# Kernel tuning notes

Measured on AMD Instinct MI355X. Metric: run time of the kernel, lower is better.

## Reference

```python
import jax, jax.numpy as jnp
import numpy as np

NP, NA, H, K, TAU = 4096, 2048, 128, 5, 1.0
NODE_N = {'paper': NP, 'author': NA}
RELS = [('pp', 'paper', 'paper'), ('aa', 'author', 'author'),
        ('pa', 'paper', 'author'), ('ap', 'author', 'paper')]


def setup_inputs():
    key = jax.random.key(0)
    ks = jax.random.split(key, 32)
    f32 = jnp.float32
    def nrm(k, shape, scale=1.0):
        return jax.random.normal(k, shape, f32) * scale
    Epp, Eaa, Epa, Eap = 131072, 65536, 131072, 131072
    inp = {
        'x_paper': nrm(ks[0], (NP, H)),
        'x_author': nrm(ks[1], (NA, H)),
        'ei_pp': jax.random.randint(ks[2], (2, Epp), 0, NP, dtype=jnp.int32),
        'ei_aa': jax.random.randint(ks[3], (2, Eaa), 0, NA, dtype=jnp.int32),
        'ei_pa': jnp.stack([jax.random.randint(ks[4], (Epa,), 0, NP, dtype=jnp.int32),
                            jax.random.randint(ks[5], (Epa,), 0, NA, dtype=jnp.int32)]),
        'ei_ap': jnp.stack([jax.random.randint(ks[6], (Eap,), 0, NA, dtype=jnp.int32),
                            jax.random.randint(ks[7], (Eap,), 0, NP, dtype=jnp.int32)]),
        'batch_paper': jnp.zeros((NP,), jnp.int32),
        'batch_author': jnp.zeros((NA,), jnp.int32),
        'index': 7,
    }
    s = H ** -0.5
    i = 8
    for t in ('paper', 'author'):
        for l in (0, 1):
            inp['Wself_%s%d' % (t, l)] = nrm(ks[i], (H, H), s); i += 1
    for r, _, _ in RELS:
        for l in (0, 1):
            inp['W%s%d' % (r, l)] = nrm(ks[i], (H, H), s); i += 1
    for r in ('pp', 'aa'):
        inp['Wep1_%s' % r] = nrm(ks[i], (2 * H, 256), (2 * H) ** -0.5); i += 1
        inp['bep1_%s' % r] = jnp.zeros((256,), f32)
        inp['Wep2_%s' % r] = nrm(ks[i], (256, 2), 256 ** -0.5); i += 1
        inp['bep2_%s' % r] = jnp.zeros((2,), f32)
    inp['Wc'] = nrm(ks[i], (H, 5), s)
    inp['bc'] = jnp.zeros((5,), f32)
    return inp


def _mean_agg(msg, dst, n):
    s = jax.ops.segment_sum(msg, dst, num_segments=n)
    c = jax.ops.segment_sum(jnp.ones((msg.shape[0], 1), msg.dtype), dst, num_segments=n)
    return s / jnp.maximum(c, 1.0)


def _gnn(x, ei, p, single, edge_attn=None):
    # 2-layer relation-typed mean-aggregation hetero GNN.
    h = dict(x)
    for l in (0, 1):
        nh = {}
        for t in ('paper', 'author'):
            agg = h[t] @ p['Wself_%s%d' % (t, l)]
            for r, s_t, d_t in RELS:
                if d_t != t or (single and s_t != d_t):
                    continue
                src, dst = ei[r][0], ei[r][1]
                msg = h[s_t][src] @ p['W%s%d' % (r, l)]  # [E, H]
                if edge_attn is not None and r in edge_attn:
                    msg = msg * edge_attn[r][:, None]
                agg = agg + _mean_agg(msg, dst, NODE_N[t])
            nh[t] = jax.nn.relu(agg)
        h = nh
    return h


def _edge_pred(h, ei, p, r, t):
    src, dst = ei[r][0], ei[r][1]
    e = jnp.concatenate([h[t][src], h[t][dst]], axis=-1)  # [E, 2H]
    e = jax.nn.relu(e @ p['Wep1_%s' % r] + p['bep1_%s' % r])
    return e @ p['Wep2_%s' % r] + p['bep2_%s' % r]  # [E, 2]


def _gumbel_topk(logits, mask, k, tau, key):
    # Masked straight-through top-k gumbel-softmax (row-wise, hard=True).
    u = jax.random.uniform(key, logits.shape, logits.dtype, 1e-10, 1.0)
    g = -jnp.log(-jnp.log(u))
    y = jnp.where(mask, (logits + g) / tau, -1e9)
    soft = jax.nn.softmax(y, axis=-1)
    _, idx = jax.lax.top_k(soft, k)  # [N, k]
    rows = jnp.arange(logits.shape[0])[:, None]
    hard = jnp.zeros_like(soft).at[rows, idx].set(1.0)
    return hard - jax.lax.stop_gradient(soft) + soft


def _prune(h, ei, p, r, t, n, key):
    pred = _edge_pred(h, ei, p, r, t)[:, 0]
    src, dst = ei[r][0], ei[r][1]
    # sparse_coo_tensor(...).to_dense(): duplicates coalesce by sum
    A = jnp.zeros((n, n), pred.dtype).at[src, dst].add(pred)
    S = _gumbel_topk(A, A > 0, K, TAU, key)
    return S[src, dst]


def _forward(p, ints):
    x = {'paper': p['x_paper'], 'author': p['x_author']}
    ei = {'pp': ints['ei_pp'], 'aa': ints['ei_aa'], 'pa': ints['ei_pa'], 'ap': ints['ei_ap']}
    h1 = _gnn(x, ei, p, single=True)
    kpp, kaa = jax.random.split(jax.random.key(42))
    w_pp = _prune(h1, ei, p, 'pp', 'paper', NP, kpp)
    w_aa = _prune(h1, ei, p, 'aa', 'author', NA, kaa)
    h2 = _gnn(x, ei, p, single=False, edge_attn={'pp': w_pp, 'aa': w_aa})
    pool = h2['paper'][ints['index']].reshape(1, -1)
    y_hat = pool @ p['Wc'] + p['bc']
    return y_hat, w_pp, w_aa


def reference(x_paper, x_author, ei_pp, ei_aa, ei_pa, ei_ap, batch_paper, batch_author, index,
              Wself_paper0, Wself_paper1, Wself_author0, Wself_author1,
              Wpp0, Wpp1, Waa0, Waa1, Wpa0, Wpa1, Wap0, Wap1,
              Wep1_pp, bep1_pp, Wep2_pp, bep2_pp, Wep1_aa, bep1_aa, Wep2_aa, bep2_aa,
              Wc, bc):
    p = dict(x_paper=x_paper, x_author=x_author,
             Wself_paper0=Wself_paper0, Wself_paper1=Wself_paper1,
             Wself_author0=Wself_author0, Wself_author1=Wself_author1,
             Wpp0=Wpp0, Wpp1=Wpp1, Waa0=Waa0, Waa1=Waa1,
             Wpa0=Wpa0, Wpa1=Wpa1, Wap0=Wap0, Wap1=Wap1,
             Wep1_pp=Wep1_pp, bep1_pp=bep1_pp, Wep2_pp=Wep2_pp, bep2_pp=bep2_pp,
             Wep1_aa=Wep1_aa, bep1_aa=bep1_aa, Wep2_aa=Wep2_aa, bep2_aa=bep2_aa,
             Wc=Wc, bc=bc)
    ints = dict(ei_pp=ei_pp, ei_aa=ei_aa, ei_pa=ei_pa, ei_ap=ei_ap, index=index)
    return _forward(p, ints)
```

## Files before the change

kernel.cpp:

```cpp
#include <hip/hip_runtime.h>
#include <stdint.h>


namespace {

constexpr int NPn = 4096;
constexpr int NAn = 2048;
constexpr int Hh  = 128;
constexpr int EPPc = 131072;
constexpr int EAAc = 65536;
constexpr int KSEL = 5;
constexpr int BSLOT = 128;


__host__ __device__ static inline void tf2x32(uint32_t k0, uint32_t k1,
                                              uint32_t& x0, uint32_t& x1) {
  uint32_t ks2 = k0 ^ k1 ^ 0x1BD11BDAu;
  x0 += k0; x1 += k1;
#define TF_R(r) { x0 += x1; x1 = (x1 << (r)) | (x1 >> (32 - (r))); x1 ^= x0; }
  TF_R(13) TF_R(15) TF_R(26) TF_R(6)
  x0 += k1;  x1 += ks2 + 1u;
  TF_R(17) TF_R(29) TF_R(16) TF_R(24)
  x0 += ks2; x1 += k0 + 2u;
  TF_R(13) TF_R(15) TF_R(26) TF_R(6)
  x0 += k0;  x1 += k1 + 3u;
  TF_R(17) TF_R(29) TF_R(16) TF_R(24)
  x0 += k1;  x1 += ks2 + 4u;
  TF_R(13) TF_R(15) TF_R(26) TF_R(6)
  x0 += ks2; x1 += k0 + 5u;
#undef TF_R
}

__global__ __launch_bounds__(256) void scatter_kernel(
    const int* src_pp, const int* dst_pp, const int* src_aa, const int* dst_aa,
    const int* src_pa, const int* dst_pa, const int* src_ap, const int* dst_ap,
    int* cnt, int* entries)
{
  int i = blockIdx.x * 256 + threadIdx.x;
  int key, pl;
  if (i < 131072) {
    int e = i;
    key = 0 + dst_pp[e]; pl = (src_pp[e] << 18) | e;
  } else if (i < 196608) {
    int e = i - 131072;
    key = 4096 + dst_aa[e]; pl = (src_aa[e] << 16) | e;
  } else if (i < 327680) {
    int e = i - 196608;
    key = 6144 + dst_pa[e]; pl = src_pa[e];
  } else if (i < 458752) {
    int e = i - 327680;
    key = 8192 + dst_ap[e]; pl = src_ap[e];
  } else if (i < 589824) {
    int e = i - 458752;
    key = 12288 + src_pp[e]; pl = (dst_pp[e] << 18) | e;
  } else if (i < 655360) {
    int e = i - 589824;
    key = 16384 + src_aa[e]; pl = (dst_aa[e] << 16) | e;
  } else return;
  int pos = atomicAdd(&cnt[key], 1);
  if (pos < BSLOT) entries[key * BSLOT + pos] = pl;
}

struct FDesc {
  const float* gsrc; const float* wArr; int cntOff; int shift;
  float* Mout;
  const float* Aself; const float* W0; const float* W1;
  const float* A2;  const float* W2;
  float* C; int relu;
  const float* WP; float* P1; float* P2;
};
struct FArgs { FDesc d[4]; int bstart[5]; int nd; };

__global__ __launch_bounds__(256) void fused_layer(FArgs fa, const int* __restrict__ cnt,
                                                   const int* __restrict__ entries)
{
  __shared__ __align__(16) float Ms[8][128];
  __shared__ __align__(16) float Xs[8][128];
  __shared__ __align__(16) float Zs[8][128];
  __shared__ __align__(16) float Ws[32][128];
  int blk = blockIdx.x, tid = threadIdx.x;
  int di = 0;
  while (di < fa.nd - 1 && blk >= fa.bstart[di + 1]) ++di;
  FDesc D = fa.d[di];
  int node0 = (blk - fa.bstart[di]) * 8;
  {
    int hw = tid >> 5;
    int node = node0 + hw;
    int fl = (tid & 31) << 2;
    int deg = cnt[D.cntOff + node];
    const int* ent = entries + (size_t)(D.cntOff + node) * BSLOT;
    const float* h = D.gsrc;
    int sh = D.shift;
    float ax = 0.f, ay = 0.f, az = 0.f, aw = 0.f;
    if (D.wArr) {
      unsigned mask = (1u << sh) - 1u;
      int k = 0;
      for (; k + 3 < deg; k += 4) {
        unsigned p0 = (unsigned)ent[k], p1 = (unsigned)ent[k + 1];
        unsigned p2 = (unsigned)ent[k + 2], p3 = (unsigned)ent[k + 3];
        float w0 = D.wArr[p0 & mask], w1 = D.wArr[p1 & mask];
        float w2v = D.wArr[p2 & mask], w3 = D.wArr[p3 & mask];
        float4 v0, v1, v2, v3;
        if (w0 != 0.f) v0 = *(const float4*)&h[(size_t)(p0 >> sh) * Hh + fl];
        if (w1 != 0.f) v1 = *(const float4*)&h[(size_t)(p1 >> sh) * Hh + fl];
        if (w2v != 0.f) v2 = *(const float4*)&h[(size_t)(p2 >> sh) * Hh + fl];
        if (w3 != 0.f) v3 = *(const float4*)&h[(size_t)(p3 >> sh) * Hh + fl];
        if (w0 != 0.f) { ax += v0.x; ay += v0.y; az += v0.z; aw += v0.w; }
        if (w1 != 0.f) { ax += v1.x; ay += v1.y; az += v1.z; aw += v1.w; }
        if (w2v != 0.f) { ax += v2.x; ay += v2.y; az += v2.z; aw += v2.w; }
        if (w3 != 0.f) { ax += v3.x; ay += v3.y; az += v3.z; aw += v3.w; }
      }
      for (; k < deg; ++k) {
        unsigned pl = (unsigned)ent[k];
        float wt = D.wArr[pl & mask];
        if (wt != 0.f) {
          float4 v = *(const float4*)&h[(size_t)(pl >> sh) * Hh + fl];
          ax += v.x; ay += v.y; az += v.z; aw += v.w;
        }
      }
    } else {
      int k = 0;
      for (; k + 7 < deg; k += 8) {
        unsigned p0 = (unsigned)ent[k],     p1 = (unsigned)ent[k + 1];
        unsigned p2 = (unsigned)ent[k + 2], p3 = (unsigned)ent[k + 3];
        unsigned p4 = (unsigned)ent[k + 4], p5 = (unsigned)ent[k + 5];
        unsigned p6 = (unsigned)ent[k + 6], p7 = (unsigned)ent[k + 7];
        float4 v0 = *(const float4*)&h[(size_t)(p0 >> sh) * Hh + fl];
        float4 v1 = *(const float4*)&h[(size_t)(p1 >> sh) * Hh + fl];
        float4 v2 = *(const float4*)&h[(size_t)(p2 >> sh) * Hh + fl];
        float4 v3 = *(const float4*)&h[(size_t)(p3 >> sh) * Hh + fl];
        float4 v4 = *(const float4*)&h[(size_t)(p4 >> sh) * Hh + fl];
        float4 v5 = *(const float4*)&h[(size_t)(p5 >> sh) * Hh + fl];
        float4 v6 = *(const float4*)&h[(size_t)(p6 >> sh) * Hh + fl];
        float4 v7 = *(const float4*)&h[(size_t)(p7 >> sh) * Hh + fl];
        ax += v0.x; ay += v0.y; az += v0.z; aw += v0.w;
        ax += v1.x; ay += v1.y; az += v1.z; aw += v1.w;
        ax += v2.x; ay += v2.y; az += v2.z; aw += v2.w;
        ax += v3.x; ay += v3.y; az += v3.z; aw += v3.w;
        ax += v4.x; ay += v4.y; az += v4.z; aw += v4.w;
        ax += v5.x; ay += v5.y; az += v5.z; aw += v5.w;
        ax += v6.x; ay += v6.y; az += v6.z; aw += v6.w;
        ax += v7.x; ay += v7.y; az += v7.z; aw += v7.w;
      }
      for (; k < deg; ++k) {
        unsigned pl = (unsigned)ent[k];
        float4 v = *(const float4*)&h[(size_t)(pl >> sh) * Hh + fl];
        ax += v.x; ay += v.y; az += v.z; aw += v.w;
      }
    }
    float cd = fmaxf((float)deg, 1.0f);
    float4 o; o.x = ax / cd; o.y = ay / cd; o.z = az / cd; o.w = aw / cd;
    if (D.W0 == nullptr) {
      *(float4*)&D.Mout[(size_t)node * Hh + fl] = o;
    } else {
      *(float4*)&Ms[hw][fl] = o;
    }
  }
  if (D.W0 == nullptr) return;
  {
    int rm = tid >> 5, cq = (tid & 31) << 2;
    *(float4*)&Xs[rm][cq] = *(const float4*)&D.Aself[(size_t)(node0 + rm) * 128 + cq];
    if (D.A2)
      *(float4*)&Zs[rm][cq] = *(const float4*)&D.A2[(size_t)(node0 + rm) * 128 + cq];
  }
  int m = tid >> 5, nq = tid & 31;
  float4 accv = {0.f, 0.f, 0.f, 0.f};
  int parts = D.A2 ? 3 : 2;
  for (int p = 0; p < parts; ++p) {
    const float* W = (p == 0) ? D.W0 : (p == 1) ? D.W1 : D.W2;
    for (int c = 0; c < 4; ++c) {
      __syncthreads();
      {
        int r = tid >> 3, f = (tid & 7) << 4;
        const float* srcp = &W[(size_t)(c * 32 + r) * 128 + f];
        *(float4*)&Ws[r][f]      = *(const float4*)&srcp[0];
        *(float4*)&Ws[r][f + 4]  = *(const float4*)&srcp[4];
        *(float4*)&Ws[r][f + 8]  = *(const float4*)&srcp[8];
        *(float4*)&Ws[r][f + 12] = *(const float4*)&srcp[12];
      }
      __syncthreads();
#define KCHUNK(AR)                                              \
      _Pragma("unroll")                                         \
      for (int k = 0; k < 32; ++k) {                            \
        float a = AR[m][c * 32 + k];                            \
        float4 wv = *(const float4*)&Ws[k][nq << 2];            \
        accv.x += a * wv.x; accv.y += a * wv.y;                 \
        accv.z += a * wv.z; accv.w += a * wv.w;                 \
      }
      if (p == 0) { KCHUNK(Xs) } else if (p == 1) { KCHUNK(Ms) } else { KCHUNK(Zs) }
#undef KCHUNK
    }
  }
  if (D.relu) {
    accv.x = fmaxf(accv.x, 0.f); accv.y = fmaxf(accv.y, 0.f);
    accv.z = fmaxf(accv.z, 0.f); accv.w = fmaxf(accv.w, 0.f);
  }
  if (D.C)
    *(float4*)&D.C[(size_t)(node0 + m) * 128 + (nq << 2)] = accv;
  if (D.WP == nullptr) return;
  __syncthreads();
  *(float4*)&Xs[m][nq << 2] = accv;
  __syncthreads();
  {
    int half = tid >> 7;
    int rg = (tid >> 6) & 1;
    int c0 = (tid & 63) << 2;
    const float* Wb = D.WP + ((size_t)(half ? 128 : 0)) * 256 + c0;
    float4 acc0 = {0,0,0,0}, acc1 = {0,0,0,0}, acc2 = {0,0,0,0}, acc3 = {0,0,0,0};
    for (int k = 0; k < 128; k += 2) {
      float4 w0 = *(const float4*)&Wb[(size_t)k * 256];
      float4 w1 = *(const float4*)&Wb[(size_t)(k + 1) * 256];
      float2 a0 = *(const float2*)&Xs[rg * 4 + 0][k];
      float2 a1 = *(const float2*)&Xs[rg * 4 + 1][k];
      float2 a2 = *(const float2*)&Xs[rg * 4 + 2][k];
      float2 a3 = *(const float2*)&Xs[rg * 4 + 3][k];
      acc0.x += a0.x * w0.x; acc0.y += a0.x * w0.y; acc0.z += a0.x * w0.z; acc0.w += a0.x * w0.w;
      acc0.x += a0.y * w1.x; acc0.y += a0.y * w1.y; acc0.z += a0.y * w1.z; acc0.w += a0.y * w1.w;
      acc1.x += a1.x * w0.x; acc1.y += a1.x * w0.y; acc1.z += a1.x * w0.z; acc1.w += a1.x * w0.w;
      acc1.x += a1.y * w1.x; acc1.y += a1.y * w1.y; acc1.z += a1.y * w1.z; acc1.w += a1.y * w1.w;
      acc2.x += a2.x * w0.x; acc2.y += a2.x * w0.y; acc2.z += a2.x * w0.z; acc2.w += a2.x * w0.w;
      acc2.x += a2.y * w1.x; acc2.y += a2.y * w1.y; acc2.z += a2.y * w1.z; acc2.w += a2.y * w1.w;
      acc3.x += a3.x * w0.x; acc3.y += a3.x * w0.y; acc3.z += a3.x * w0.z; acc3.w += a3.x * w0.w;
      acc3.x += a3.y * w1.x; acc3.y += a3.y * w1.y; acc3.z += a3.y * w1.z; acc3.w += a3.y * w1.w;
    }
    float* Pout = half ? D.P2 : D.P1;
    *(float4*)&Pout[(size_t)(node0 + rg * 4 + 0) * 256 + c0] = acc0;
    *(float4*)&Pout[(size_t)(node0 + rg * 4 + 1) * 256 + c0] = acc1;
    *(float4*)&Pout[(size_t)(node0 + rg * 4 + 2) * 256 + c0] = acc2;
    *(float4*)&Pout[(size_t)(node0 + rg * 4 + 3) * 256 + c0] = acc3;
  }
}

__global__ __launch_bounds__(256) void row_topk(
    const float* __restrict__ P1pp, const float* __restrict__ P2pp,
    const float* __restrict__ b1pp, const float* __restrict__ W2pp,
    const float* __restrict__ b2pp,
    const float* __restrict__ P1aa, const float* __restrict__ P2aa,
    const float* __restrict__ b1aa, const float* __restrict__ W2aa,
    const float* __restrict__ b2aa,
    const int* __restrict__ cnt, const int* __restrict__ entries,
    float* __restrict__ w_pp, float* __restrict__ w_aa,
    uint32_t kpp0, uint32_t kpp1, uint32_t kaa0, uint32_t kaa1)
{
  __shared__ int   dS[4][128];
  __shared__ float pS[4][128];
  __shared__ int   sel5[4][KSEL];
  int blk = blockIdx.x, tid = threadIdx.x;
  int lane = tid & 63, wv = tid >> 6;
  int row, Ncols, shift;
  int co; unsigned mask;
  const float* P1; const float* P2; const float* b1; const float* W2; const float* b2;
  float* wout; uint32_t k0, k1;
  if (blk < NPn / 4) {
    row = blk * 4 + wv; Ncols = NPn; shift = 18; mask = 0x3FFFFu; co = 12288;
    P1 = P1pp; P2 = P2pp; b1 = b1pp; W2 = W2pp; b2 = b2pp;
    wout = w_pp; k0 = kpp0; k1 = kpp1;
  } else {
    row = (blk - NPn / 4) * 4 + wv; Ncols = NAn; shift = 16; mask = 0xFFFFu; co = 16384;
    P1 = P1aa; P2 = P2aa; b1 = b1aa; W2 = W2aa; b2 = b2aa;
    wout = w_aa; k0 = kaa0; k1 = kaa1;
  }
  const int* ent = entries + (size_t)(co + row) * BSLOT;
  int deg = cnt[co + row];
  int j = lane << 2;
  float4 p1v = *(const float4*)&P1[(size_t)row * 256 + j];
  float4 b1v = *(const float4*)&b1[j];
  float wa = W2[(j + 0) * 2], wb = W2[(j + 1) * 2];
  float wc = W2[(j + 2) * 2], wd = W2[(j + 3) * 2];
  float bias2 = b2[0];
  float pa = p1v.x, pb = p1v.y, pc = p1v.z, pd = p1v.w;
  float ba = b1v.x, bb = b1v.y, bc_ = b1v.z, bd = b1v.w;
  for (int k = 0; k < deg; k += 4) {
    int n = deg - k; if (n > 4) n = 4;
    unsigned pl0 = (unsigned)ent[k];
    unsigned pl1 = (n > 1) ? (unsigned)ent[k + 1] : pl0;
    unsigned pl2 = (n > 2) ? (unsigned)ent[k + 2] : pl0;
    unsigned pl3 = (n > 3) ? (unsigned)ent[k + 3] : pl0;
    int d0 = (int)(pl0 >> shift), d1 = (int)(pl1 >> shift);
    int d2 = (int)(pl2 >> shift), d3 = (int)(pl3 >> shift);
    float4 q0 = *(const float4*)&P2[(size_t)d0 * 256 + j];
    float4 q1 = *(const float4*)&P2[(size_t)d1 * 256 + j];
    float4 q2 = *(const float4*)&P2[(size_t)d2 * 256 + j];
    float4 q3 = *(const float4*)&P2[(size_t)d3 * 256 + j];
    float s0 = fmaxf(pa + q0.x + ba, 0.f) * wa + fmaxf(pb + q0.y + bb, 0.f) * wb +
               fmaxf(pc + q0.z + bc_, 0.f) * wc + fmaxf(pd + q0.w + bd, 0.f) * wd;
    float s1 = fmaxf(pa + q1.x + ba, 0.f) * wa + fmaxf(pb + q1.y + bb, 0.f) * wb +
               fmaxf(pc + q1.z + bc_, 0.f) * wc + fmaxf(pd + q1.w + bd, 0.f) * wd;
    float s2 = fmaxf(pa + q2.x + ba, 0.f) * wa + fmaxf(pb + q2.y + bb, 0.f) * wb +
               fmaxf(pc + q2.z + bc_, 0.f) * wc + fmaxf(pd + q2.w + bd, 0.f) * wd;
    float s3 = fmaxf(pa + q3.x + ba, 0.f) * wa + fmaxf(pb + q3.y + bb, 0.f) * wb +
               fmaxf(pc + q3.z + bc_, 0.f) * wc + fmaxf(pd + q3.w + bd, 0.f) * wd;
    for (int off = 32; off; off >>= 1) {
      s0 += __shfl_down(s0, off);
      s1 += __shfl_down(s1, off);
      s2 += __shfl_down(s2, off);
      s3 += __shfl_down(s3, off);
    }
    if (lane == 0) {
      dS[wv][k] = d0; pS[wv][k] = s0 + bias2;
      if (n > 1) { dS[wv][k + 1] = d1; pS[wv][k + 1] = s1 + bias2; }
      if (n > 2) { dS[wv][k + 2] = d2; pS[wv][k + 2] = s2 + bias2; }
      if (n > 3) { dS[wv][k + 3] = d3; pS[wv][k + 3] = s3 + bias2; }
    }
  }
  __syncthreads();
  if (deg > 0) {
    int   e0 = (lane < deg) ? dS[wv][lane] : -1;
    float q0v = (lane < deg) ? pS[wv][lane] : 0.f;
    bool  two = (deg > 64);
    int   e1 = -1; float q1v = 0.f;
    if (two && 64 + lane < deg) { e1 = dS[wv][64 + lane]; q1v = pS[wv][64 + lane]; }
    float a0 = 0.f, a1 = 0.f;
    bool lead0 = (e0 >= 0), lead1 = (e1 >= 0);
    for (int j2 = 0; j2 < deg; ++j2) {
      int bj; float bp;
      if (j2 < 64) { bj = __shfl(e0, j2); bp = __shfl(q0v, j2); }
      else         { bj = __shfl(e1, j2 - 64); bp = __shfl(q1v, j2 - 64); }
      if (e0 >= 0 && bj == e0) { a0 += bp; if (j2 < lane) lead0 = false; }
      if (e1 >= 0 && bj == e1) { a1 += bp; if (j2 < 64 + lane) lead1 = false; }
    }
    uint32_t rowbase = (uint32_t)row * (uint32_t)Ncols;
    float y0 = -1e9f, y1 = -1e9f;
    bool c0 = lead0 && (a0 > 0.f);
    if (c0) {
      uint32_t x0 = 0u, x1 = rowbase + (uint32_t)e0;
      tf2x32(k0, k1, x0, x1);
      uint32_t bits = x0 ^ x1;
      float fv = __uint_as_float((bits >> 9) | 0x3f800000u) - 1.0f;
      float u = fmaxf(1e-10f, fv + 1e-10f);
      y0 = a0 + (-logf(-logf(u)));
    }
    bool c1 = lead1 && (a1 > 0.f);
    if (c1) {
      uint32_t x0 = 0u, x1 = rowbase + (uint32_t)e1;
      tf2x32(k0, k1, x0, x1);
      uint32_t bits = x0 ^ x1;
      float fv = __uint_as_float((bits >> 9) | 0x3f800000u) - 1.0f;
      float u = fmaxf(1e-10f, fv + 1e-10f);
      y1 = a1 + (-logf(-logf(u)));
    }
    int cnt2 = __popcll(__ballot(c0)) + __popcll(__ballot(c1));
    int nsel = cnt2 < KSEL ? cnt2 : KSEL;
    for (int it = 0; it < nsel; ++it) {
      float best; int bc;
      if (y1 > y0 || (y1 == y0 && (unsigned)e1 < (unsigned)e0)) { best = y1; bc = e1; }
      else { best = y0; bc = e0; }
      for (int mm = 32; mm; mm >>= 1) {
        float ov = __shfl_xor(best, mm); int oc = __shfl_xor(bc, mm);
        if (ov > best || (ov == best && (unsigned)oc < (unsigned)bc)) { best = ov; bc = oc; }
      }
      if (lane == 0) sel5[wv][it] = bc;
      if (e0 == bc) y0 = -3.0e38f;
      if (e1 == bc) y1 = -3.0e38f;
    }
    if (nsel < KSEL && lane == 0) {
      int c = 0;
      for (int it = nsel; it < KSEL; ++it) {
// ... 77 lines not shown
{
  (void)in_sizes; (void)n_in; (void)out_size; (void)ws_size;
  const float* x_p = (const float*)d_in[0];
  const float* x_a = (const float*)d_in[1];
  const int* ei_pp = (const int*)d_in[2];
  const int* ei_aa = (const int*)d_in[3];
  const int* ei_pa = (const int*)d_in[4];
  const int* ei_ap = (const int*)d_in[5];
  const int* idxPtr = (const int*)d_in[8];
  const float* Wself_p0 = (const float*)d_in[9];
  const float* Wself_p1 = (const float*)d_in[10];
  const float* Wself_a0 = (const float*)d_in[11];
  const float* Wself_a1 = (const float*)d_in[12];
  const float* Wpp0 = (const float*)d_in[13]; const float* Wpp1 = (const float*)d_in[14];
  const float* Waa0 = (const float*)d_in[15]; const float* Waa1 = (const float*)d_in[16];
  const float* Wpa0 = (const float*)d_in[17];
  const float* Wap0 = (const float*)d_in[19]; const float* Wap1 = (const float*)d_in[20];
  const float* Wep1_pp = (const float*)d_in[21]; const float* bep1_pp = (const float*)d_in[22];
  const float* Wep2_pp = (const float*)d_in[23]; const float* bep2_pp = (const float*)d_in[24];
  const float* Wep1_aa = (const float*)d_in[25]; const float* bep1_aa = (const float*)d_in[26];
  const float* Wep2_aa = (const float*)d_in[27]; const float* bep2_aa = (const float*)d_in[28];
  const float* Wc = (const float*)d_in[29]; const float* bc = (const float*)d_in[30];

  float* out = (float*)d_out;
  float* w_pp_out = out + 5;
  float* w_aa_out = out + 5 + EPPc;

  const int* src_pp = ei_pp;  const int* dst_pp = ei_pp + EPPc;
  const int* src_aa = ei_aa;  const int* dst_aa = ei_aa + EAAc;
  const int* src_pa = ei_pa;  const int* dst_pa = ei_pa + 131072;
  const int* src_ap = ei_ap;  const int* dst_ap = ei_ap + 131072;

  char* p = (char*)d_ws;
  auto alloc = [&](size_t bytes) -> void* {
    void* r = (void*)p;
    p += (bytes + 255) & ~(size_t)255;
    return r;
  };
  int* cnt     = (int*)alloc(18432 * sizeof(int));
  int* entries = (int*)alloc((size_t)18432 * BSLOT * sizeof(int));
  float* Map  = (float*)alloc((size_t)NPn * Hh * sizeof(float));
  float* Mpa  = (float*)alloc((size_t)NAn * Hh * sizeof(float));
  float* h1p0 = (float*)alloc((size_t)NPn * Hh * sizeof(float));
  float* h1a0 = (float*)alloc((size_t)NAn * Hh * sizeof(float));
  float* h2p0 = (float*)alloc((size_t)NPn * Hh * sizeof(float));
  float* h2a0 = (float*)alloc((size_t)NAn * Hh * sizeof(float));
  float* P1pp = (float*)alloc((size_t)NPn * 256 * sizeof(float));
  float* P2pp = (float*)alloc((size_t)NPn * 256 * sizeof(float));
  float* P1aa = (float*)alloc((size_t)NAn * 256 * sizeof(float));
  float* P2aa = (float*)alloc((size_t)NAn * 256 * sizeof(float));

  const int CO_PPD = 0, CO_AAD = 4096, CO_PAD = 6144, CO_APD = 8192;

  hipMemsetAsync(cnt, 0, 18432 * sizeof(int), stream);
  scatter_kernel<<<2560, 256, 0, stream>>>(src_pp, dst_pp, src_aa, dst_aa,
                                           src_pa, dst_pa, src_ap, dst_ap,
                                           cnt, entries);

  {
    FArgs fa{};
    fa.d[0] = {x_p, nullptr, CO_PPD, 18, nullptr,
               x_p, Wself_p0, Wpp0, nullptr, nullptr, h1p0, 1,
               nullptr, nullptr, nullptr};
    fa.d[1] = {x_a, nullptr, CO_AAD, 16, nullptr,
               x_a, Wself_a0, Waa0, nullptr, nullptr, h1a0, 1,
               nullptr, nullptr, nullptr};
    fa.d[2] = {x_a, nullptr, CO_APD, 0, Map,
               nullptr, nullptr, nullptr, nullptr, nullptr, nullptr, 0,
               nullptr, nullptr, nullptr};
    fa.d[3] = {x_p, nullptr, CO_PAD, 0, Mpa,
               nullptr, nullptr, nullptr, nullptr, nullptr, nullptr, 0,
               nullptr, nullptr, nullptr};
    fa.bstart[0] = 0; fa.bstart[1] = 512; fa.bstart[2] = 768;
    fa.bstart[3] = 1280; fa.bstart[4] = 1536; fa.nd = 4;
    fused_layer<<<1536, 256, 0, stream>>>(fa, cnt, entries);
  }

  {
    FArgs fa{};
    fa.d[0] = {h1p0, nullptr, CO_PPD, 18, nullptr,
               h1p0, Wself_p1, Wpp1, nullptr, nullptr, nullptr, 1,
               Wep1_pp, P1pp, P2pp};
    fa.d[1] = {h1a0, nullptr, CO_AAD, 16, nullptr,
               h1a0, Wself_a1, Waa1, nullptr, nullptr, nullptr, 1,
               Wep1_aa, P1aa, P2aa};
    fa.bstart[0] = 0; fa.bstart[1] = 512; fa.bstart[2] = 768; fa.nd = 2;
    fused_layer<<<768, 256, 0, stream>>>(fa, cnt, entries);
  }

  uint32_t kpp0, kpp1, kaa0, kaa1;
  { uint32_t a0 = 0, a1 = 0; tf2x32(0u, 42u, a0, a1); kpp0 = a0; kpp1 = a1; }
  { uint32_t a0 = 0, a1 = 1; tf2x32(0u, 42u, a0, a1); kaa0 = a0; kaa1 = a1; }

  row_topk<<<(NPn + NAn) / 4, 256, 0, stream>>>(P1pp, P2pp, bep1_pp, Wep2_pp, bep2_pp,
                                                P1aa, P2aa, bep1_aa, Wep2_aa, bep2_aa,
                                                cnt, entries, w_pp_out, w_aa_out,
                                                kpp0, kpp1, kaa0, kaa1);

  {
    FArgs fa{};
    fa.d[0] = {x_p, w_pp_out, CO_PPD, 18, nullptr,
               x_p, Wself_p0, Wpp0, Map, Wap0, h2p0, 1,
               nullptr, nullptr, nullptr};
    fa.d[1] = {x_a, w_aa_out, CO_AAD, 16, nullptr,
               x_a, Wself_a0, Waa0, Mpa, Wpa0, h2a0, 1,
               nullptr, nullptr, nullptr};
    fa.bstart[0] = 0; fa.bstart[1] = 512; fa.bstart[2] = 768; fa.nd = 2;
    fused_layer<<<768, 256, 0, stream>>>(fa, cnt, entries);
  }

  final_kernel<<<1, 128, 0, stream>>>(h2p0, h2a0, idxPtr, w_pp_out,
                                      cnt, entries,
                                      Wself_p1, Wpp1, Wap1, Wc, bc, out);
}
```

Baseline: 325.6 us.

## Process 16 nodes per GEMM block and widen top-k scoring to 8 edges

GEMM-bearing blocks of the fused layer now handle 16 nodes instead of 8. Each thread computes two output rows per weight tile, so every weight tile loaded into shared memory is reused across twice as many rows. Shared memory moves to a dynamically sized buffer so the Z tile is only allocated when needed, and grid sizes and block offsets are recomputed to match. The row_topk scoring loop now scores 8 edges per iteration instead of 4 to expose more memory-level parallelism. The trade-off is fewer blocks per launch (384 for the GEMM layers), which lowers occupancy and latency hiding for the gather phase, plus higher register pressure.

```diff
diff --git a/kernel.cpp b/kernel.cpp
--- a/kernel.cpp
+++ b/kernel.cpp
@@ -74,97 +74,107 @@
 __global__ __launch_bounds__(256) void fused_layer(FArgs fa, const int* __restrict__ cnt,
                                                    const int* __restrict__ entries)
 {
-  __shared__ __align__(16) float Ms[8][128];
-  __shared__ __align__(16) float Xs[8][128];
-  __shared__ __align__(16) float Zs[8][128];
-  __shared__ __align__(16) float Ws[32][128];
+  extern __shared__ __align__(16) float lds[];
+  float (*Xs)[128] = (float (*)[128])(lds);
+  float (*Ms)[128] = (float (*)[128])(lds + 16 * 128);
+  float (*Ws)[128] = (float (*)[128])(lds + 32 * 128);
+  float (*Zs)[128] = (float (*)[128])(lds + 64 * 128);
   int blk = blockIdx.x, tid = threadIdx.x;
   int di = 0;
   while (di < fa.nd - 1 && blk >= fa.bstart[di + 1]) ++di;
   FDesc D = fa.d[di];
-  int node0 = (blk - fa.bstart[di]) * 8;
+  bool isGemm = (D.W0 != nullptr);
+  int node0 = (blk - fa.bstart[di]) * (isGemm ? 16 : 8);
   {
     int hw = tid >> 5;
-    int node = node0 + hw;
     int fl = (tid & 31) << 2;
-    int deg = cnt[D.cntOff + node];
-    const int* ent = entries + (size_t)(D.cntOff + node) * BSLOT;
-    const float* h = D.gsrc;
-    int sh = D.shift;
-    float ax = 0.f, ay = 0.f, az = 0.f, aw = 0.f;
-    if (D.wArr) {
-      unsigned mask = (1u << sh) - 1u;
-      int k = 0;
-      for (; k + 3 < deg; k += 4) {
-        unsigned p0 = (unsigned)ent[k], p1 = (unsigned)ent[k + 1];
-        unsigned p2 = (unsigned)ent[k + 2], p3 = (unsigned)ent[k + 3];
-        float w0 = D.wArr[p0 & mask], w1 = D.wArr[p1 & mask];
-        float w2v = D.wArr[p2 & mask], w3 = D.wArr[p3 & mask];
-        float4 v0, v1, v2, v3;
-        if (w0 != 0.f) v0 = *(const float4*)&h[(size_t)(p0 >> sh) * Hh + fl];
-        if (w1 != 0.f) v1 = *(const float4*)&h[(size_t)(p1 >> sh) * Hh + fl];
-        if (w2v != 0.f) v2 = *(const float4*)&h[(size_t)(p2 >> sh) * Hh + fl];
-        if (w3 != 0.f) v3 = *(const float4*)&h[(size_t)(p3 >> sh) * Hh + fl];
-        if (w0 != 0.f) { ax += v0.x; ay += v0.y; az += v0.z; aw += v0.w; }
-        if (w1 != 0.f) { ax += v1.x; ay += v1.y; az += v1.z; aw += v1.w; }
-        if (w2v != 0.f) { ax += v2.x; ay += v2.y; az += v2.z; aw += v2.w; }
-        if (w3 != 0.f) { ax += v3.x; ay += v3.y; az += v3.z; aw += v3.w; }
-      }
-      for (; k < deg; ++k) {
-        unsigned pl = (unsigned)ent[k];
-        float wt = D.wArr[pl & mask];
-        if (wt != 0.f) {
+    int npass = isGemm ? 2 : 1;
+    for (int ps = 0; ps < npass; ++ps) {
+      int node = node0 + ps * 8 + hw;
+      int deg = cnt[D.cntOff + node];
+      const int* ent = entries + (size_t)(D.cntOff + node) * BSLOT;
+      const float* h = D.gsrc;
+      int sh = D.shift;
+      float ax = 0.f, ay = 0.f, az = 0.f, aw = 0.f;
+      if (D.wArr) {
+        unsigned mask = (1u << sh) - 1u;
+        int k = 0;
+        for (; k + 3 < deg; k += 4) {
+          unsigned p0 = (unsigned)ent[k], p1 = (unsigned)ent[k + 1];
+          unsigned p2 = (unsigned)ent[k + 2], p3 = (unsigned)ent[k + 3];
+          float w0 = D.wArr[p0 & mask], w1 = D.wArr[p1 & mask];
+          float w2v = D.wArr[p2 & mask], w3 = D.wArr[p3 & mask];
+          float4 v0, v1, v2, v3;
+          if (w0 != 0.f) v0 = *(const float4*)&h[(size_t)(p0 >> sh) * Hh + fl];
+          if (w1 != 0.f) v1 = *(const float4*)&h[(size_t)(p1 >> sh) * Hh + fl];
+          if (w2v != 0.f) v2 = *(const float4*)&h[(size_t)(p2 >> sh) * Hh + fl];
+          if (w3 != 0.f) v3 = *(const float4*)&h[(size_t)(p3 >> sh) * Hh + fl];
+          if (w0 != 0.f) { ax += v0.x; ay += v0.y; az += v0.z; aw += v0.w; }
+          if (w1 != 0.f) { ax += v1.x; ay += v1.y; az += v1.z; aw += v1.w; }
+          if (w2v != 0.f) { ax += v2.x; ay += v2.y; az += v2.z; aw += v2.w; }
+          if (w3 != 0.f) { ax += v3.x; ay += v3.y; az += v3.z; aw += v3.w; }
+        }
+        for (; k < deg; ++k) {
+          unsigned pl = (unsigned)ent[k];
+          float wt = D.wArr[pl & mask];
+          if (wt != 0.f) {
+            float4 v = *(const float4*)&h[(size_t)(pl >> sh) * Hh + fl];
+            ax += v.x; ay += v.y; az += v.z; aw += v.w;
+          }
+        }
+      } else {
+        int k = 0;
+        for (; k + 7 < deg; k += 8) {
+          unsigned p0 = (unsigned)ent[k],     p1 = (unsigned)ent[k + 1];
+          unsigned p2 = (unsigned)ent[k + 2], p3 = (unsigned)ent[k + 3];
+          unsigned p4 = (unsigned)ent[k + 4], p5 = (unsigned)ent[k + 5];
+          unsigned p6 = (unsigned)ent[k + 6], p7 = (unsigned)ent[k + 7];
+          float4 v0 = *(const float4*)&h[(size_t)(p0 >> sh) * Hh + fl];
+          float4 v1 = *(const float4*)&h[(size_t)(p1 >> sh) * Hh + fl];
+          float4 v2 = *(const float4*)&h[(size_t)(p2 >> sh) * Hh + fl];
+          float4 v3 = *(const float4*)&h[(size_t)(p3 >> sh) * Hh + fl];
+          float4 v4 = *(const float4*)&h[(size_t)(p4 >> sh) * Hh + fl];
+          float4 v5 = *(const float4*)&h[(size_t)(p5 >> sh) * Hh + fl];
+          float4 v6 = *(const float4*)&h[(size_t)(p6 >> sh) * Hh + fl];
+          float4 v7 = *(const float4*)&h[(size_t)(p7 >> sh) * Hh + fl];
+          ax += v0.x; ay += v0.y; az += v0.z; aw += v0.w;
+          ax += v1.x; ay += v1.y; az += v1.z; aw += v1.w;
+          ax += v2.x; ay += v2.y; az += v2.z; aw += v2.w;
+          ax += v3.x; ay += v3.y; az += v3.z; aw += v3.w;
+          ax += v4.x; ay += v4.y; az += v4.z; aw += v4.w;
+          ax += v5.x; ay += v5.y; az += v5.z; aw += v5.w;
+          ax += v6.x; ay += v6.y; az += v6.z; aw += v6.w;
+          ax += v7.x; ay += v7.y; az += v7.z; aw += v7.w;
+        }
+        for (; k < deg; ++k) {
+          unsigned pl = (unsigned)ent[k];
           float4 v = *(const float4*)&h[(size_t)(pl >> sh) * Hh + fl];
           ax += v.x; ay += v.y; az += v.z; aw += v.w;
         }
       }
-    } else {
-      int k = 0;
-      for (; k + 7 < deg; k += 8) {
-        unsigned p0 = (unsigned)ent[k],     p1 = (unsigned)ent[k + 1];
-        unsigned p2 = (unsigned)ent[k + 2], p3 = (unsigned)ent[k + 3];
-        unsigned p4 = (unsigned)ent[k + 4], p5 = (unsigned)ent[k + 5];
-        unsigned p6 = (unsigned)ent[k + 6], p7 = (unsigned)ent[k + 7];
-        float4 v0 = *(const float4*)&h[(size_t)(p0 >> sh) * Hh + fl];
-        float4 v1 = *(const float4*)&h[(size_t)(p1 >> sh) * Hh + fl];
-        float4 v2 = *(const float4*)&h[(size_t)(p2 >> sh) * Hh + fl];
-        float4 v3 = *(const float4*)&h[(size_t)(p3 >> sh) * Hh + fl];
-        float4 v4 = *(const float4*)&h[(size_t)(p4 >> sh) * Hh + fl];
-        float4 v5 = *(const float4*)&h[(size_t)(p5 >> sh) * Hh + fl];
-        float4 v6 = *(const float4*)&h[(size_t)(p6 >> sh) * Hh + fl];
-        float4 v7 = *(const float4*)&h[(size_t)(p7 >> sh) * Hh + fl];
-        ax += v0.x; ay += v0.y; az += v0.z; aw += v0.w;
-        ax += v1.x; ay += v1.y; az += v1.z; aw += v1.w;
-        ax += v2.x; ay += v2.y; az += v2.z; aw += v2.w;
-        ax += v3.x; ay += v3.y; az += v3.z; aw += v3.w;
-        ax += v4.x; ay += v4.y; az += v4.z; aw += v4.w;
-        ax += v5.x; ay += v5.y; az += v5.z; aw += v5.w;
-        ax += v6.x; ay += v6.y; az += v6.z; aw += v6.w;
-        ax += v7.x; ay += v7.y; az += v7.z; aw += v7.w;
-      }
-      for (; k < deg; ++k) {
-        unsigned pl = (unsigned)ent[k];
-        float4 v = *(const float4*)&h[(size_t)(pl >> sh) * Hh + fl];
-        ax += v.x; ay += v.y; az += v.z; aw += v.w;
-      }
-    }
-    float cd = fmaxf((float)deg, 1.0f);
-    float4 o; o.x = ax / cd; o.y = ay / cd; o.z = az / cd; o.w = aw / cd;
-    if (D.W0 == nullptr) {
-      *(float4*)&D.Mout[(size_t)node * Hh + fl] = o;
-    } else {
-      *(float4*)&Ms[hw][fl] = o;
-    }
-  }
-  if (D.W0 == nullptr) return;
-  {
-    int rm = tid >> 5, cq = (tid & 31) << 2;
-    *(float4*)&Xs[rm][cq] = *(const float4*)&D.Aself[(size_t)(node0 + rm) * 128 + cq];
-    if (D.A2)
-      *(float4*)&Zs[rm][cq] = *(const float4*)&D.A2[(size_t)(node0 + rm) * 128 + cq];
-  }
-  int m = tid >> 5, nq = tid & 31;
-  float4 accv = {0.f, 0.f, 0.f, 0.f};
+      float cd = fmaxf((float)deg, 1.0f);
+      float4 o; o.x = ax / cd; o.y = ay / cd; o.z = az / cd; o.w = aw / cd;
+      if (!isGemm) {
+        *(float4*)&D.Mout[(size_t)node * Hh + fl] = o;
+      } else {
+        *(float4*)&Ms[ps * 8 + hw][fl] = o;
+      }
+    }
+  }
+  if (!isGemm) return;
+  {
+    int cq = (tid & 31) << 2;
+    for (int q = 0; q < 2; ++q) {
+      int rm = (tid >> 5) + q * 8;
+      *(float4*)&Xs[rm][cq] = *(const float4*)&D.Aself[(size_t)(node0 + rm) * 128 + cq];
+      if (D.A2)
+        *(float4*)&Zs[rm][cq] = *(const float4*)&D.A2[(size_t)(node0 + rm) * 128 + cq];
+    }
+  }
+  int rg = tid >> 5, nq = tid & 31;
+  int r0 = rg * 2;
+  float4 acc0 = {0.f, 0.f, 0.f, 0.f};
+  float4 acc1 = {0.f, 0.f, 0.f, 0.f};
   int parts = D.A2 ? 3 : 2;
   for (int p = 0; p < parts; ++p) {
     const float* W = (p == 0) ? D.W0 : (p == 1) ? D.W1 : D.W2;
@@ -182,52 +192,63 @@
 #define KCHUNK(AR)                                              \
       _Pragma("unroll")                                         \
       for (int k = 0; k < 32; ++k) {                            \
-        float a = AR[m][c * 32 + k];                            \
         float4 wv = *(const float4*)&Ws[k][nq << 2];            \
-        accv.x += a * wv.x; accv.y += a * wv.y;                 \
-        accv.z += a * wv.z; accv.w += a * wv.w;                 \
+        float a0 = AR[r0][c * 32 + k];                          \
+        float a1 = AR[r0 + 1][c * 32 + k];                      \
+        acc0.x += a0 * wv.x; acc0.y += a0 * wv.y;               \
+        acc0.z += a0 * wv.z; acc0.w += a0 * wv.w;               \
+        acc1.x += a1 * wv.x; acc1.y += a1 * wv.y;               \
+        acc1.z += a1 * wv.z; acc1.w += a1 * wv.w;               \
       }
       if (p == 0) { KCHUNK(Xs) } else if (p == 1) { KCHUNK(Ms) } else { KCHUNK(Zs) }
 #undef KCHUNK
     }
   }
   if (D.relu) {
-    accv.x = fmaxf(accv.x, 0.f); accv.y = fmaxf(accv.y, 0.f);
-    accv.z = fmaxf(accv.z, 0.f); accv.w = fmaxf(accv.w, 0.f);
-  }
-  if (D.C)
-    *(float4*)&D.C[(size_t)(node0 + m) * 128 + (nq << 2)] = accv;
+    acc0.x = fmaxf(acc0.x, 0.f); acc0.y = fmaxf(acc0.y, 0.f);
+    acc0.z = fmaxf(acc0.z, 0.f); acc0.w = fmaxf(acc0.w, 0.f);
+    acc1.x = fmaxf(acc1.x, 0.f); acc1.y = fmaxf(acc1.y, 0.f);
+    acc1.z = fmaxf(acc1.z, 0.f); acc1.w = fmaxf(acc1.w, 0.f);
+  }
+  if (D.C) {
+    *(float4*)&D.C[(size_t)(node0 + r0) * 128 + (nq << 2)]     = acc0;
+    *(float4*)&D.C[(size_t)(node0 + r0 + 1) * 128 + (nq << 2)] = acc1;
+  }
   if (D.WP == nullptr) return;
   __syncthreads();
-  *(float4*)&Xs[m][nq << 2] = accv;
+  *(float4*)&Xs[r0][nq << 2]     = acc0;
+  *(float4*)&Xs[r0 + 1][nq << 2] = acc1;
   __syncthreads();
   {
     int half = tid >> 7;
-    int rg = (tid >> 6) & 1;
+    int rgp = (tid >> 6) & 1;
     int c0 = (tid & 63) << 2;
     const float* Wb = D.WP + ((size_t)(half ? 128 : 0)) * 256 + c0;
-    float4 acc0 = {0,0,0,0}, acc1 = {0,0,0,0}, acc2 = {0,0,0,0}, acc3 = {0,0,0,0};
-    for (int k = 0; k < 128; k += 2) {
-      float4 w0 = *(const float4*)&Wb[(size_t)k * 256];
-      float4 w1 = *(const float4*)&Wb[(size_t)(k + 1) * 256];
-      float2 a0 = *(const float2*)&Xs[rg * 4 + 0][k];
-      float2 a1 = *(const float2*)&Xs[rg * 4 + 1][k];
-      float2 a2 = *(const float2*)&Xs[rg * 4 + 2][k];
-      float2 a3 = *(const float2*)&Xs[rg * 4 + 3][k];
-      acc0.x += a0.x * w0.x; acc0.y += a0.x * w0.y; acc0.z += a0.x * w0.z; acc0.w += a0.x * w0.w;
-      acc0.x += a0.y * w1.x; acc0.y += a0.y * w1.y; acc0.z += a0.y * w1.z; acc0.w += a0.y * w1.w;
-      acc1.x += a1.x * w0.x; acc1.y += a1.x * w0.y; acc1.z += a1.x * w0.z; acc1.w += a1.x * w0.w;
-      acc1.x += a1.y * w1.x; acc1.y += a1.y * w1.y; acc1.z += a1.y * w1.z; acc1.w += a1.y * w1.w;
-      acc2.x += a2.x * w0.x; acc2.y += a2.x * w0.y; acc2.z += a2.x * w0.z; acc2.w += a2.x * w0.w;
-      acc2.x += a2.y * w1.x; acc2.y += a2.y * w1.y; acc2.z += a2.y * w1.z; acc2.w += a2.y * w1.w;
-      acc3.x += a3.x * w0.x; acc3.y += a3.x * w0.y; acc3.z += a3.x * w0.z; acc3.w += a3.x * w0.w;
-      acc3.x += a3.y * w1.x; acc3.y += a3.y * w1.y; acc3.z += a3.y * w1.z; acc3.w += a3.y * w1.w;
-    }
     float* Pout = half ? D.P2 : D.P1;
-    *(float4*)&Pout[(size_t)(node0 + rg * 4 + 0) * 256 + c0] = acc0;
-    *(float4*)&Pout[(size_t)(node0 + rg * 4 + 1) * 256 + c0] = acc1;
-    *(float4*)&Pout[(size_t)(node0 + rg * 4 + 2) * 256 + c0] = acc2;
-    *(float4*)&Pout[(size_t)(node0 + rg * 4 + 3) * 256 + c0] = acc3;
+    for (int q = 0; q < 2; ++q) {
+      int rb = q * 8 + rgp * 4;
+      float4 a_0 = {0,0,0,0}, a_1 = {0,0,0,0}, a_2 = {0,0,0,0}, a_3 = {0,0,0,0};
+      for (int k = 0; k < 128; k += 2) {
+        float4 w0 = *(const float4*)&Wb[(size_t)k * 256];
+        float4 w1 = *(const float4*)&Wb[(size_t)(k + 1) * 256];
+        float2 x0 = *(const float2*)&Xs[rb + 0][k];
+        float2 x1 = *(const float2*)&Xs[rb + 1][k];
+        float2 x2 = *(const float2*)&Xs[rb + 2][k];
+        float2 x3 = *(const float2*)&Xs[rb + 3][k];
+        a_0.x += x0.x * w0.x; a_0.y += x0.x * w0.y; a_0.z += x0.x * w0.z; a_0.w += x0.x * w0.w;
+        a_0.x += x0.y * w1.x; a_0.y += x0.y * w1.y; a_0.z += x0.y * w1.z; a_0.w += x0.y * w1.w;
+        a_1.x += x1.x * w0.x; a_1.y += x1.x * w0.y; a_1.z += x1.x * w0.z; a_1.w += x1.x * w0.w;
+        a_1.x += x1.y * w1.x; a_1.y += x1.y * w1.y; a_1.z += x1.y * w1.z; a_1.w += x1.y * w1.w;
+        a_2.x += x2.x * w0.x; a_2.y += x2.x * w0.y; a_2.z += x2.x * w0.z; a_2.w += x2.x * w0.w;
+        a_2.x += x2.y * w1.x; a_2.y += x2.y * w1.y; a_2.z += x2.y * w1.z; a_2.w += x2.y * w1.w;
+        a_3.x += x3.x * w0.x; a_3.y += x3.x * w0.y; a_3.z += x3.x * w0.z; a_3.w += x3.x * w0.w;
+        a_3.x += x3.y * w1.x; a_3.y += x3.y * w1.y; a_3.z += x3.y * w1.z; a_3.w += x3.y * w1.w;
+      }
+      *(float4*)&Pout[(size_t)(node0 + rb + 0) * 256 + c0] = a_0;
+      *(float4*)&Pout[(size_t)(node0 + rb + 1) * 256 + c0] = a_1;
+      *(float4*)&Pout[(size_t)(node0 + rb + 2) * 256 + c0] = a_2;
+      *(float4*)&Pout[(size_t)(node0 + rb + 3) * 256 + c0] = a_3;
+    }
   }
 }
 
@@ -270,39 +291,54 @@
   float bias2 = b2[0];
   float pa = p1v.x, pb = p1v.y, pc = p1v.z, pd = p1v.w;
   float ba = b1v.x, bb = b1v.y, bc_ = b1v.z, bd = b1v.w;
-  for (int k = 0; k < deg; k += 4) {
-    int n = deg - k; if (n > 4) n = 4;
+#define SCORE(q) (fmaxf(pa + q.x + ba, 0.f) * wa + fmaxf(pb + q.y + bb, 0.f) * wb + \
+                  fmaxf(pc + q.z + bc_, 0.f) * wc + fmaxf(pd + q.w + bd, 0.f) * wd)
+  for (int k = 0; k < deg; k += 8) {
+    int n = deg - k; if (n > 8) n = 8;
     unsigned pl0 = (unsigned)ent[k];
     unsigned pl1 = (n > 1) ? (unsigned)ent[k + 1] : pl0;
     unsigned pl2 = (n > 2) ? (unsigned)ent[k + 2] : pl0;
     unsigned pl3 = (n > 3) ? (unsigned)ent[k + 3] : pl0;
+    unsigned pl4 = (n > 4) ? (unsigned)ent[k + 4] : pl0;
+    unsigned pl5 = (n > 5) ? (unsigned)ent[k + 5] : pl0;
+    unsigned pl6 = (n > 6) ? (unsigned)ent[k + 6] : pl0;
+    unsigned pl7 = (n > 7) ? (unsigned)ent[k + 7] : pl0;
     int d0 = (int)(pl0 >> shift), d1 = (int)(pl1 >> shift);
     int d2 = (int)(pl2 >> shift), d3 = (int)(pl3 >> shift);
+    int d4 = (int)(pl4 >> shift), d5 = (int)(pl5 >> shift);
+    int d6 = (int)(pl6 >> shift), d7 = (int)(pl7 >> shift);
     float4 q0 = *(const float4*)&P2[(size_t)d0 * 256 + j];
     float4 q1 = *(const float4*)&P2[(size_t)d1 * 256 + j];
     float4 q2 = *(const float4*)&P2[(size_t)d2 * 256 + j];
     float4 q3 = *(const float4*)&P2[(size_t)d3 * 256 + j];
-    float s0 = fmaxf(pa + q0.x + ba, 0.f) * wa + fmaxf(pb + q0.y + bb, 0.f) * wb +
-               fmaxf(pc + q0.z + bc_, 0.f) * wc + fmaxf(pd + q0.w + bd, 0.f) * wd;
-    float s1 = fmaxf(pa + q1.x + ba, 0.f) * wa + fmaxf(pb + q1.y + bb, 0.f) * wb +
-               fmaxf(pc + q1.z + bc_, 0.f) * wc + fmaxf(pd + q1.w + bd, 0.f) * wd;
-    float s2 = fmaxf(pa + q2.x + ba, 0.f) * wa + fmaxf(pb + q2.y + bb, 0.f) * wb +
-               fmaxf(pc + q2.z + bc_, 0.f) * wc + fmaxf(pd + q2.w + bd, 0.f) * wd;
-    float s3 = fmaxf(pa + q3.x + ba, 0.f) * wa + fmaxf(pb + q3.y + bb, 0.f) * wb +
-               fmaxf(pc + q3.z + bc_, 0.f) * wc + fmaxf(pd + q3.w + bd, 0.f) * wd;
+    float4 q4 = *(const float4*)&P2[(size_t)d4 * 256 + j];
+    float4 q5 = *(const float4*)&P2[(size_t)d5 * 256 + j];
+    float4 q6 = *(const float4*)&P2[(size_t)d6 * 256 + j];
+    float4 q7 = *(const float4*)&P2[(size_t)d7 * 256 + j];
+    float s0 = SCORE(q0), s1 = SCORE(q1), s2 = SCORE(q2), s3 = SCORE(q3);
+    float s4 = SCORE(q4), s5 = SCORE(q5), s6 = SCORE(q6), s7 = SCORE(q7);
     for (int off = 32; off; off >>= 1) {
       s0 += __shfl_down(s0, off);
       s1 += __shfl_down(s1, off);
       s2 += __shfl_down(s2, off);
       s3 += __shfl_down(s3, off);
+      s4 += __shfl_down(s4, off);
+      s5 += __shfl_down(s5, off);
+      s6 += __shfl_down(s6, off);
+      s7 += __shfl_down(s7, off);
     }
     if (lane == 0) {
       dS[wv][k] = d0; pS[wv][k] = s0 + bias2;
       if (n > 1) { dS[wv][k + 1] = d1; pS[wv][k + 1] = s1 + bias2; }
       if (n > 2) { dS[wv][k + 2] = d2; pS[wv][k + 2] = s2 + bias2; }
       if (n > 3) { dS[wv][k + 3] = d3; pS[wv][k + 3] = s3 + bias2; }
-    }
-  }
+      if (n > 4) { dS[wv][k + 4] = d4; pS[wv][k + 4] = s4 + bias2; }
+      if (n > 5) { dS[wv][k + 5] = d5; pS[wv][k + 5] = s5 + bias2; }
+      if (n > 6) { dS[wv][k + 6] = d6; pS[wv][k + 6] = s6 + bias2; }
+      if (n > 7) { dS[wv][k + 7] = d7; pS[wv][k + 7] = s7 + bias2; }
+    }
+  }
+#undef SCORE
   __syncthreads();
   if (deg > 0) {
     int   e0 = (lane < deg) ? dS[wv][lane] : -1;
@@ -486,6 +522,9 @@
 
   const int CO_PPD = 0, CO_AAD = 4096, CO_PAD = 6144, CO_APD = 8192;
 
+  const size_t SH_NOZ = (size_t)64 * 128 * sizeof(float);
+  const size_t SH_Z   = (size_t)80 * 128 * sizeof(float);
+
   hipMemsetAsync(cnt, 0, 18432 * sizeof(int), stream);
   scatter_kernel<<<2560, 256, 0, stream>>>(src_pp, dst_pp, src_aa, dst_aa,
                                            src_pa, dst_pa, src_ap, dst_ap,
@@ -505,9 +544,9 @@
     fa.d[3] = {x_p, nullptr, CO_PAD, 0, Mpa,
                nullptr, nullptr, nullptr, nullptr, nullptr, nullptr, 0,
                nullptr, nullptr, nullptr};
-    fa.bstart[0] = 0; fa.bstart[1] = 512; fa.bstart[2] = 768;
-    fa.bstart[3] = 1280; fa.bstart[4] = 1536; fa.nd = 4;
-    fused_layer<<<1536, 256, 0, stream>>>(fa, cnt, entries);
+    fa.bstart[0] = 0; fa.bstart[1] = 256; fa.bstart[2] = 384;
+    fa.bstart[3] = 896; fa.bstart[4] = 1152; fa.nd = 4;
+    fused_layer<<<1152, 256, SH_NOZ, stream>>>(fa, cnt, entries);
   }
 
   {
@@ -518,8 +557,8 @@
     fa.d[1] = {h1a0, nullptr, CO_AAD, 16, nullptr,
                h1a0, Wself_a1, Waa1, nullptr, nullptr, nullptr, 1,
                Wep1_aa, P1aa, P2aa};
-    fa.bstart[0] = 0; fa.bstart[1] = 512; fa.bstart[2] = 768; fa.nd = 2;
-    fused_layer<<<768, 256, 0, stream>>>(fa, cnt, entries);
+    fa.bstart[0] = 0; fa.bstart[1] = 256; fa.bstart[2] = 384; fa.nd = 2;
+    fused_layer<<<384, 256, SH_NOZ, stream>>>(fa, cnt, entries);
   }
 
   uint32_t kpp0, kpp1, kaa0, kaa1;
@@ -539,8 +578,8 @@
     fa.d[1] = {x_a, w_aa_out, CO_AAD, 16, nullptr,
                x_a, Wself_a0, Waa0, Mpa, Wpa0, h2a0, 1,
                nullptr, nullptr, nullptr};
-    fa.bstart[0] = 0; fa.bstart[1] = 512; fa.bstart[2] = 768; fa.nd = 2;
-    fused_layer<<<768, 256, 0, stream>>>(fa, cnt, entries);
+    fa.bstart[0] = 0; fa.bstart[1] = 256; fa.bstart[2] = 384; fa.nd = 2;
+    fused_layer<<<384, 256, SH_Z, stream>>>(fa, cnt, entries);
   }
 
   final_kernel<<<1, 128, 0, stream>>>(h2p0, h2a0, idxPtr, w_pp_out,
```

New measurement: 342.4 us. 5.2% more time.

## Read weights directly from global in fused layer GEMM; widen edge-score batch to 8

Applied to the files above, without the earlier changes.

The per-node transform GEMM no longer stages 32-row weight chunks in shared memory behind two barriers per chunk. Each thread now reads float4 weight columns straight from global/L2 and float4 activations from shared memory, which removes the synchronisation and cuts shared memory per block. In exchange, every block re-reads the full weight matrices from cache. Separately, the edge-predictor scoring loop handles 8 neighbours per iteration instead of 4, adding memory-level parallelism for the gathered P2 loads at the cost of more registers.

```diff
diff --git a/kernel.cpp b/kernel.cpp
--- a/kernel.cpp
+++ b/kernel.cpp
@@ -74,10 +74,9 @@
 __global__ __launch_bounds__(256) void fused_layer(FArgs fa, const int* __restrict__ cnt,
                                                    const int* __restrict__ entries)
 {
+  __shared__ __align__(16) float Xs[8][128];
   __shared__ __align__(16) float Ms[8][128];
-  __shared__ __align__(16) float Xs[8][128];
   __shared__ __align__(16) float Zs[8][128];
-  __shared__ __align__(16) float Ws[32][128];
   int blk = blockIdx.x, tid = threadIdx.x;
   int di = 0;
   while (di < fa.nd - 1 && blk >= fa.bstart[di + 1]) ++di;
@@ -163,33 +162,32 @@
     if (D.A2)
       *(float4*)&Zs[rm][cq] = *(const float4*)&D.A2[(size_t)(node0 + rm) * 128 + cq];
   }
+  __syncthreads();
   int m = tid >> 5, nq = tid & 31;
   float4 accv = {0.f, 0.f, 0.f, 0.f};
   int parts = D.A2 ? 3 : 2;
   for (int p = 0; p < parts; ++p) {
     const float* W = (p == 0) ? D.W0 : (p == 1) ? D.W1 : D.W2;
-    for (int c = 0; c < 4; ++c) {
-      __syncthreads();
-      {
-        int r = tid >> 3, f = (tid & 7) << 4;
-        const float* srcp = &W[(size_t)(c * 32 + r) * 128 + f];
-        *(float4*)&Ws[r][f]      = *(const float4*)&srcp[0];
-        *(float4*)&Ws[r][f + 4]  = *(const float4*)&srcp[4];
-        *(float4*)&Ws[r][f + 8]  = *(const float4*)&srcp[8];
-        *(float4*)&Ws[r][f + 12] = *(const float4*)&srcp[12];
-      }
-      __syncthreads();
-#define KCHUNK(AR)                                              \
-      _Pragma("unroll")                                         \
-      for (int k = 0; k < 32; ++k) {                            \
-        float a = AR[m][c * 32 + k];                            \
-        float4 wv = *(const float4*)&Ws[k][nq << 2];            \
-        accv.x += a * wv.x; accv.y += a * wv.y;                 \
-        accv.z += a * wv.z; accv.w += a * wv.w;                 \
-      }
-      if (p == 0) { KCHUNK(Xs) } else if (p == 1) { KCHUNK(Ms) } else { KCHUNK(Zs) }
-#undef KCHUNK
-    }
+    const float* Wc_ = W + (nq << 2);
+#define KPART(AR)                                                   \
+    _Pragma("unroll 2")                                             \
+    for (int k = 0; k < 128; k += 4) {                              \
+      float4 av = *(const float4*)&AR[m][k];                        \
+      float4 w0 = *(const float4*)&Wc_[(size_t)(k + 0) * 128];      \
+      float4 w1 = *(const float4*)&Wc_[(size_t)(k + 1) * 128];      \
+      float4 w2 = *(const float4*)&Wc_[(size_t)(k + 2) * 128];      \
+      float4 w3 = *(const float4*)&Wc_[(size_t)(k + 3) * 128];      \
+      accv.x += av.x * w0.x; accv.y += av.x * w0.y;                 \
+      accv.z += av.x * w0.z; accv.w += av.x * w0.w;                 \
+      accv.x += av.y * w1.x; accv.y += av.y * w1.y;                 \
+      accv.z += av.y * w1.z; accv.w += av.y * w1.w;                 \
+      accv.x += av.z * w2.x; accv.y += av.z * w2.y;                 \
+      accv.z += av.z * w2.z; accv.w += av.z * w2.w;                 \
+      accv.x += av.w * w3.x; accv.y += av.w * w3.y;                 \
+      accv.z += av.w * w3.z; accv.w += av.w * w3.w;                 \
+    }
+    if (p == 0) { KPART(Xs) } else if (p == 1) { KPART(Ms) } else { KPART(Zs) }
+#undef KPART
   }
   if (D.relu) {
     accv.x = fmaxf(accv.x, 0.f); accv.y = fmaxf(accv.y, 0.f);
@@ -270,39 +268,54 @@
   float bias2 = b2[0];
   float pa = p1v.x, pb = p1v.y, pc = p1v.z, pd = p1v.w;
   float ba = b1v.x, bb = b1v.y, bc_ = b1v.z, bd = b1v.w;
-  for (int k = 0; k < deg; k += 4) {
-    int n = deg - k; if (n > 4) n = 4;
+#define SCORE(q) (fmaxf(pa + q.x + ba, 0.f) * wa + fmaxf(pb + q.y + bb, 0.f) * wb + \
+                  fmaxf(pc + q.z + bc_, 0.f) * wc + fmaxf(pd + q.w + bd, 0.f) * wd)
+  for (int k = 0; k < deg; k += 8) {
+    int n = deg - k; if (n > 8) n = 8;
     unsigned pl0 = (unsigned)ent[k];
     unsigned pl1 = (n > 1) ? (unsigned)ent[k + 1] : pl0;
     unsigned pl2 = (n > 2) ? (unsigned)ent[k + 2] : pl0;
     unsigned pl3 = (n > 3) ? (unsigned)ent[k + 3] : pl0;
+    unsigned pl4 = (n > 4) ? (unsigned)ent[k + 4] : pl0;
+    unsigned pl5 = (n > 5) ? (unsigned)ent[k + 5] : pl0;
+    unsigned pl6 = (n > 6) ? (unsigned)ent[k + 6] : pl0;
+    unsigned pl7 = (n > 7) ? (unsigned)ent[k + 7] : pl0;
     int d0 = (int)(pl0 >> shift), d1 = (int)(pl1 >> shift);
     int d2 = (int)(pl2 >> shift), d3 = (int)(pl3 >> shift);
+    int d4 = (int)(pl4 >> shift), d5 = (int)(pl5 >> shift);
+    int d6 = (int)(pl6 >> shift), d7 = (int)(pl7 >> shift);
     float4 q0 = *(const float4*)&P2[(size_t)d0 * 256 + j];
     float4 q1 = *(const float4*)&P2[(size_t)d1 * 256 + j];
     float4 q2 = *(const float4*)&P2[(size_t)d2 * 256 + j];
     float4 q3 = *(const float4*)&P2[(size_t)d3 * 256 + j];
-    float s0 = fmaxf(pa + q0.x + ba, 0.f) * wa + fmaxf(pb + q0.y + bb, 0.f) * wb +
-               fmaxf(pc + q0.z + bc_, 0.f) * wc + fmaxf(pd + q0.w + bd, 0.f) * wd;
-    float s1 = fmaxf(pa + q1.x + ba, 0.f) * wa + fmaxf(pb + q1.y + bb, 0.f) * wb +
-               fmaxf(pc + q1.z + bc_, 0.f) * wc + fmaxf(pd + q1.w + bd, 0.f) * wd;
-    float s2 = fmaxf(pa + q2.x + ba, 0.f) * wa + fmaxf(pb + q2.y + bb, 0.f) * wb +
-               fmaxf(pc + q2.z + bc_, 0.f) * wc + fmaxf(pd + q2.w + bd, 0.f) * wd;
-    float s3 = fmaxf(pa + q3.x + ba, 0.f) * wa + fmaxf(pb + q3.y + bb, 0.f) * wb +
-               fmaxf(pc + q3.z + bc_, 0.f) * wc + fmaxf(pd + q3.w + bd, 0.f) * wd;
+    float4 q4 = *(const float4*)&P2[(size_t)d4 * 256 + j];
+    float4 q5 = *(const float4*)&P2[(size_t)d5 * 256 + j];
+    float4 q6 = *(const float4*)&P2[(size_t)d6 * 256 + j];
+    float4 q7 = *(const float4*)&P2[(size_t)d7 * 256 + j];
+    float s0 = SCORE(q0), s1 = SCORE(q1), s2 = SCORE(q2), s3 = SCORE(q3);
+    float s4 = SCORE(q4), s5 = SCORE(q5), s6 = SCORE(q6), s7 = SCORE(q7);
     for (int off = 32; off; off >>= 1) {
       s0 += __shfl_down(s0, off);
       s1 += __shfl_down(s1, off);
       s2 += __shfl_down(s2, off);
       s3 += __shfl_down(s3, off);
+      s4 += __shfl_down(s4, off);
+      s5 += __shfl_down(s5, off);
+      s6 += __shfl_down(s6, off);
+      s7 += __shfl_down(s7, off);
     }
     if (lane == 0) {
       dS[wv][k] = d0; pS[wv][k] = s0 + bias2;
       if (n > 1) { dS[wv][k + 1] = d1; pS[wv][k + 1] = s1 + bias2; }
       if (n > 2) { dS[wv][k + 2] = d2; pS[wv][k + 2] = s2 + bias2; }
       if (n > 3) { dS[wv][k + 3] = d3; pS[wv][k + 3] = s3 + bias2; }
-    }
-  }
+      if (n > 4) { dS[wv][k + 4] = d4; pS[wv][k + 4] = s4 + bias2; }
+      if (n > 5) { dS[wv][k + 5] = d5; pS[wv][k + 5] = s5 + bias2; }
+      if (n > 6) { dS[wv][k + 6] = d6; pS[wv][k + 6] = s6 + bias2; }
+      if (n > 7) { dS[wv][k + 7] = d7; pS[wv][k + 7] = s7 + bias2; }
+    }
+  }
+#undef SCORE
   __syncthreads();
   if (deg > 0) {
     int   e0 = (lane < deg) ? dS[wv][lane] : -1;
```

Result: slower. 357.7 us (+9.9%).
